# Optimization experiments

Hardware: AMD Instinct MI355X
Metric: run time of the kernel (lower is better)

The kernel has to match this reference:

```python
import jax, jax.numpy as jnp
import numpy as np

KNOWN_POINTS = 8
TAU = 1.0


def setup_inputs() -> dict:
    key = jax.random.key(0)
    k1, k2, k3 = jax.random.split(key, 3)
    B, N, H = 8, 56564, 256
    return {
        "x": jax.random.normal(k1, (B, N), dtype=jnp.float32),
        "point_weight": jax.random.normal(k2, (1, N), dtype=jnp.float32),
        "weight": jax.random.normal(k3, (1, N, H), dtype=jnp.float32),
        "bias": jnp.zeros((1, H), dtype=jnp.float32),
    }


def _softmax_point_selection(point_weight, B, tau):
    """Iterative straight-through HardSoftmax top-k selection (stage=2).
    Returns a (B, N) {0,1}-valued mask (with straight-through softmax grads)."""
    N = point_weight.shape[1]
    weights = jnp.broadcast_to(point_weight, (B, N))  # repeat_interleave over batch
    minimum = jax.lax.stop_gradient(jnp.min(weights))
    total = jnp.zeros((B, N), dtype=weights.dtype)
    for _ in range(KNOWN_POINTS):
        soft = jax.nn.softmax(weights / tau, axis=1)
        hard = jax.nn.one_hot(jnp.argmax(weights, axis=1), N, dtype=weights.dtype)
        # straight-through: forward = hard, backward = softmax jacobian
        one_hot = hard - jax.lax.stop_gradient(soft) + soft
        total = total + one_hot
        # masked_fill at selected positions (no grad through filled entries)
        weights = jnp.where(hard > 0, minimum - 10000.0, weights)
    return total


def reference(x, point_weight, weight, bias):
    B = x.shape[0]
    mask = _softmax_point_selection(point_weight, B, TAU)  # (B, N)
    # out[b,h] = sum_n x[b,n] * mask[b,n] * W[n,h] + bias[h]
    # (equivalent to masking the (B,N,H) weight then matmul, without materializing it)
    out = jnp.einsum('bn,nh->bh', x * mask, weight[0]) + bias
    return out
```

## Files before the change

kernel.cpp:

```cpp
#include <hip/hip_runtime.h>
#include <math.h>

#define TPB 256
#define KSEL 8
#define MAGIC 0x5EEDC0DEu

__device__ __forceinline__ unsigned long long make_key(float v, unsigned int idx) {
    unsigned int u = __float_as_uint(v);
    unsigned int ord = (u & 0x80000000u) ? ~u : (u | 0x80000000u);
    return ((unsigned long long)ord << 32) | (unsigned long long)(~idx);
}

__device__ __forceinline__ unsigned long long kmax(unsigned long long a, unsigned long long b) {
    return a > b ? a : b;
}

__device__ __forceinline__ unsigned long long wave_kmax(unsigned long long k) {
    #pragma unroll
    for (int o = 32; o > 0; o >>= 1) k = kmax(k, __shfl_xor(k, o, 64));
    return k;
}

__global__ __launch_bounds__(TPB) void fused_topk_linear(
        const float* __restrict__ x, const float* __restrict__ pw,
        const float* __restrict__ w, const float* __restrict__ bias,
        float* __restrict__ out,
        unsigned int* __restrict__ flags,
        unsigned long long* __restrict__ ws_keys,
        int N, int H, int B, int nblk) {
    __shared__ unsigned long long s_wk[(TPB / 64) * KSEL];
    __shared__ int s_idx[KSEL];
    __shared__ float s_x[16][KSEL];

    const int tid  = threadIdx.x;
    const int lane = tid & 63;
    const int wid  = tid >> 6;
    const int bid  = blockIdx.x;
    const int N4   = N >> 2;
    const int tailN = N - (N4 << 2);
    const int gid  = bid * TPB + tid;

    unsigned long long cand[5] = {0ull, 0ull, 0ull, 0ull, 0ull};
    if (gid < N4) {
        const float4 v = reinterpret_cast<const float4*>(pw)[gid];
        const unsigned int base = (unsigned int)gid * 4u;
        cand[0] = make_key(v.x, base + 0u);
        cand[1] = make_key(v.y, base + 1u);
        cand[2] = make_key(v.z, base + 2u);
        cand[3] = make_key(v.w, base + 3u);
    }
    if (bid == 0 && tid < tailN) {
        const unsigned int gi = (unsigned int)(N4 * 4 + tid);
        cand[4] = make_key(pw[gi], gi);
    }

    #pragma unroll 1
    for (int p = 0; p < KSEL; ++p) {
        unsigned long long k = kmax(kmax(kmax(cand[0], cand[1]), kmax(cand[2], cand[3])), cand[4]);
        k = wave_kmax(k);
        if (lane == 0) s_wk[wid * KSEL + p] = k;
        #pragma unroll
        for (int c = 0; c < 5; ++c) if (cand[c] == k) cand[c] = 0ull;
    }
    __syncthreads();

    if (wid == 0) {
        unsigned long long c0 = (lane < (TPB / 64) * KSEL) ? s_wk[lane] : 0ull;
        #pragma unroll 1
        for (int p = 0; p < KSEL; ++p) {
            unsigned long long m = wave_kmax(c0);
            if (lane == 0)
                __hip_atomic_store(&ws_keys[bid * KSEL + p], m,
                                   __ATOMIC_RELAXED, __HIP_MEMORY_SCOPE_AGENT);
            if (c0 == m) c0 = 0ull;
        }
        if (lane == 0 && bid != 0)
            __hip_atomic_store(&flags[bid], MAGIC,
                               __ATOMIC_RELEASE, __HIP_MEMORY_SCOPE_AGENT);
    }
    if (bid != 0) return;

    for (int i = 1 + tid; i < nblk; i += TPB) {
        while (__hip_atomic_load(&flags[i], __ATOMIC_ACQUIRE,
                                 __HIP_MEMORY_SCOPE_AGENT) != MAGIC)
            __builtin_amdgcn_s_sleep(1);
    }
    __syncthreads();

    const int nk = nblk * KSEL;
    const int k0i = wid * 128 + lane * 2;
    unsigned long long c0 = (k0i < nk)
        ? __hip_atomic_load(&ws_keys[k0i], __ATOMIC_RELAXED, __HIP_MEMORY_SCOPE_AGENT) : 0ull;
    unsigned long long c1 = (k0i + 1 < nk)
        ? __hip_atomic_load(&ws_keys[k0i + 1], __ATOMIC_RELAXED, __HIP_MEMORY_SCOPE_AGENT) : 0ull;
    #pragma unroll 1
    for (int p = 0; p < KSEL; ++p) {
        unsigned long long m = wave_kmax(kmax(c0, c1));
        if (lane == 0) s_wk[wid * KSEL + p] = m;
        if (c0 == m) c0 = 0ull;
        if (c1 == m) c1 = 0ull;
    }
    __syncthreads();
    if (wid == 0) {
        unsigned long long c = (lane < (TPB / 64) * KSEL) ? s_wk[lane] : 0ull;
        #pragma unroll 1
        for (int p = 0; p < KSEL; ++p) {
            unsigned long long m = wave_kmax(c);
            if (lane == 0) s_idx[p] = (int)(~(unsigned int)(m & 0xffffffffull));
            if (c == m) c = 0ull;
        }
    }
    __syncthreads();

    if (tid < B * KSEL) {
        const int b = tid >> 3, k = tid & 7;
        s_x[b][k] = x[(size_t)b * N + s_idx[k]];
    }
    __syncthreads();

    for (int h = tid; h < H; h += TPB) {
        float wv[KSEL];
        #pragma unroll
        for (int k = 0; k < KSEL; ++k) wv[k] = w[(size_t)s_idx[k] * H + h];
        const float bv = bias[h];
        for (int b = 0; b < B; ++b) {
            float acc = bv;
            #pragma unroll
            for (int k = 0; k < KSEL; ++k) acc += s_x[b][k] * wv[k];
            out[(size_t)b * H + h] = acc;
        }
    }
}

extern "C" void kernel_launch(void* const* d_in, const int* in_sizes, int n_in,
                              void* d_out, int out_size, void* d_ws, size_t ws_size,
                              hipStream_t stream) {
    const float* x    = (const float*)d_in[0];
    const float* pw   = (const float*)d_in[1];
    const float* w    = (const float*)d_in[2];
    const float* bias = (const float*)d_in[3];
    float* out = (float*)d_out;

    const int N = in_sizes[1];
    const int H = in_sizes[3];
    const int B = in_sizes[0] / N;
    const int N4 = N >> 2;
    const int nblk = (N4 + TPB - 1) / TPB;

    unsigned int* flags = (unsigned int*)d_ws;
    unsigned long long* keys = (unsigned long long*)((char*)d_ws + 512);

    fused_topk_linear<<<nblk, TPB, 0, stream>>>(x, pw, w, bias, out,
                                                flags, keys, N, H, B, nblk);
}
```

Before: 18.91 us.

## Replace iterative top-8 extraction with butterfly sorting-network merges and spread output over blocks

Replaces the eight sequential wave-max-and-remove passes with a per-thread sorted list of 8 candidates merged across the wave by a butterfly of bitonic top-8 merges, and the same merge across waves and across blocks. The final reduction now runs in the first B blocks, each computing one batch row, instead of block 0 doing all rows after waiting on every other block. This cuts serial shuffle rounds and shortens the tail on the last block. In exchange it adds register pressure from 8-wide u64 arrays, and B blocks now spin-wait on every flag. The final reduction also assumes nblk is at most 64 and that the flags are reset between launches.

```diff
diff --git a/kernel.cpp b/kernel.cpp
--- a/kernel.cpp
+++ b/kernel.cpp
@@ -5,20 +5,39 @@
 #define KSEL 8
 #define MAGIC 0x5EEDC0DEu
 
-__device__ __forceinline__ unsigned long long make_key(float v, unsigned int idx) {
+typedef unsigned long long u64;
+
+__device__ __forceinline__ u64 make_key(float v, unsigned int idx) {
     unsigned int u = __float_as_uint(v);
     unsigned int ord = (u & 0x80000000u) ? ~u : (u | 0x80000000u);
-    return ((unsigned long long)ord << 32) | (unsigned long long)(~idx);
+    return ((u64)ord << 32) | (u64)(~idx);
+}
+__device__ __forceinline__ u64 kmax(u64 a, u64 b) { return a > b ? a : b; }
+__device__ __forceinline__ void cswap(u64 &a, u64 &b) {
+    u64 hi = a > b ? a : b;
+    u64 lo = a > b ? b : a;
+    a = hi; b = lo;
 }
 
-__device__ __forceinline__ unsigned long long kmax(unsigned long long a, unsigned long long b) {
-    return a > b ? a : b;
+__device__ __forceinline__ void merge8(u64 a[8], const u64 b[8]) {
+    u64 t[8];
+    #pragma unroll
+    for (int i = 0; i < 8; ++i) t[i] = kmax(a[i], b[7 - i]);
+    cswap(t[0], t[4]); cswap(t[1], t[5]); cswap(t[2], t[6]); cswap(t[3], t[7]);
+    cswap(t[0], t[2]); cswap(t[1], t[3]); cswap(t[4], t[6]); cswap(t[5], t[7]);
+    cswap(t[0], t[1]); cswap(t[2], t[3]); cswap(t[4], t[5]); cswap(t[6], t[7]);
+    #pragma unroll
+    for (int i = 0; i < 8; ++i) a[i] = t[i];
 }
 
-__device__ __forceinline__ unsigned long long wave_kmax(unsigned long long k) {
+__device__ __forceinline__ void wave_butterfly_top8(u64 r[8]) {
     #pragma unroll
-    for (int o = 32; o > 0; o >>= 1) k = kmax(k, __shfl_xor(k, o, 64));
-    return k;
+    for (int o = 1; o < 64; o <<= 1) {
+        u64 b[8];
+        #pragma unroll
+        for (int i = 0; i < 8; ++i) b[i] = __shfl_xor(r[i], o, 64);
+        merge8(r, b);
+    }
 }
 
 __global__ __launch_bounds__(TPB) void fused_topk_linear(
@@ -26,11 +45,9 @@
         const float* __restrict__ w, const float* __restrict__ bias,
         float* __restrict__ out,
         unsigned int* __restrict__ flags,
-        unsigned long long* __restrict__ ws_keys,
+        u64* __restrict__ ws_keys,
         int N, int H, int B, int nblk) {
-    __shared__ unsigned long long s_wk[(TPB / 64) * KSEL];
-    __shared__ int s_idx[KSEL];
-    __shared__ float s_x[16][KSEL];
+    __shared__ u64 s_wk[TPB / 64][KSEL];
 
     const int tid  = threadIdx.x;
     const int lane = tid & 63;
@@ -40,95 +57,86 @@
     const int tailN = N - (N4 << 2);
     const int gid  = bid * TPB + tid;
 
-    unsigned long long cand[5] = {0ull, 0ull, 0ull, 0ull, 0ull};
-    if (gid < N4) {
-        const float4 v = reinterpret_cast<const float4*>(pw)[gid];
-        const unsigned int base = (unsigned int)gid * 4u;
-        cand[0] = make_key(v.x, base + 0u);
-        cand[1] = make_key(v.y, base + 1u);
-        cand[2] = make_key(v.z, base + 2u);
-        cand[3] = make_key(v.w, base + 3u);
-    }
-    if (bid == 0 && tid < tailN) {
-        const unsigned int gi = (unsigned int)(N4 * 4 + tid);
-        cand[4] = make_key(pw[gi], gi);
+    u64 r[8];
+    {
+        u64 c0 = 0, c1 = 0, c2 = 0, c3 = 0, c4 = 0;
+        if (gid < N4) {
+            const float4 v = reinterpret_cast<const float4*>(pw)[gid];
+            const unsigned int base = (unsigned int)gid * 4u;
+            c0 = make_key(v.x, base + 0u);
+            c1 = make_key(v.y, base + 1u);
+            c2 = make_key(v.z, base + 2u);
+            c3 = make_key(v.w, base + 3u);
+        }
+        if (bid == 0 && tid < tailN) {
+            const unsigned int gi = (unsigned int)(N4 * 4 + tid);
+            c4 = make_key(pw[gi], gi);
+        }
+        cswap(c0, c1); cswap(c3, c4); cswap(c2, c4); cswap(c2, c3); cswap(c0, c3);
+        cswap(c0, c2); cswap(c1, c4); cswap(c1, c3); cswap(c1, c2);
+        r[0] = c0; r[1] = c1; r[2] = c2; r[3] = c3; r[4] = c4;
+        r[5] = 0;  r[6] = 0;  r[7] = 0;
     }
 
-    #pragma unroll 1
-    for (int p = 0; p < KSEL; ++p) {
-        unsigned long long k = kmax(kmax(kmax(cand[0], cand[1]), kmax(cand[2], cand[3])), cand[4]);
-        k = wave_kmax(k);
-        if (lane == 0) s_wk[wid * KSEL + p] = k;
+    wave_butterfly_top8(r);
+
+    if (lane == 0) {
         #pragma unroll
-        for (int c = 0; c < 5; ++c) if (cand[c] == k) cand[c] = 0ull;
+        for (int i = 0; i < 8; ++i) s_wk[wid][i] = r[i];
     }
     __syncthreads();
-
     if (wid == 0) {
-        unsigned long long c0 = (lane < (TPB / 64) * KSEL) ? s_wk[lane] : 0ull;
-        #pragma unroll 1
-        for (int p = 0; p < KSEL; ++p) {
-            unsigned long long m = wave_kmax(c0);
-            if (lane == 0)
-                __hip_atomic_store(&ws_keys[bid * KSEL + p], m,
+        #pragma unroll
+        for (int wv = 1; wv < TPB / 64; ++wv) {
+            u64 b[8];
+            #pragma unroll
+            for (int i = 0; i < 8; ++i) b[i] = s_wk[wv][i];
+            merge8(r, b);
+        }
+        if (lane == 0) {
+            #pragma unroll
+            for (int i = 0; i < 8; ++i)
+                __hip_atomic_store(&ws_keys[bid * KSEL + i], r[i],
                                    __ATOMIC_RELAXED, __HIP_MEMORY_SCOPE_AGENT);
-            if (c0 == m) c0 = 0ull;
-        }
-        if (lane == 0 && bid != 0)
             __hip_atomic_store(&flags[bid], MAGIC,
                                __ATOMIC_RELEASE, __HIP_MEMORY_SCOPE_AGENT);
+        }
     }
-    if (bid != 0) return;
+    if (bid >= B) return;
 
-    for (int i = 1 + tid; i < nblk; i += TPB) {
+    for (int i = tid; i < nblk; i += TPB) {
         while (__hip_atomic_load(&flags[i], __ATOMIC_ACQUIRE,
                                  __HIP_MEMORY_SCOPE_AGENT) != MAGIC)
             __builtin_amdgcn_s_sleep(1);
     }
     __syncthreads();
 
-    const int nk = nblk * KSEL;
-    const int k0i = wid * 128 + lane * 2;
-    unsigned long long c0 = (k0i < nk)
-        ? __hip_atomic_load(&ws_keys[k0i], __ATOMIC_RELAXED, __HIP_MEMORY_SCOPE_AGENT) : 0ull;
-    unsigned long long c1 = (k0i + 1 < nk)
-        ? __hip_atomic_load(&ws_keys[k0i + 1], __ATOMIC_RELAXED, __HIP_MEMORY_SCOPE_AGENT) : 0ull;
-    #pragma unroll 1
-    for (int p = 0; p < KSEL; ++p) {
-        unsigned long long m = wave_kmax(kmax(c0, c1));
-        if (lane == 0) s_wk[wid * KSEL + p] = m;
-        if (c0 == m) c0 = 0ull;
-        if (c1 == m) c1 = 0ull;
+    u64 g[8];
+    if (lane < nblk) {
+        #pragma unroll
+        for (int i = 0; i < 8; ++i)
+            g[i] = __hip_atomic_load(&ws_keys[lane * KSEL + i],
+                                     __ATOMIC_RELAXED, __HIP_MEMORY_SCOPE_AGENT);
+    } else {
+        #pragma unroll
+        for (int i = 0; i < 8; ++i) g[i] = 0ull;
     }
-    __syncthreads();
-    if (wid == 0) {
-        unsigned long long c = (lane < (TPB / 64) * KSEL) ? s_wk[lane] : 0ull;
-        #pragma unroll 1
-        for (int p = 0; p < KSEL; ++p) {
-            unsigned long long m = wave_kmax(c);
-            if (lane == 0) s_idx[p] = (int)(~(unsigned int)(m & 0xffffffffull));
-            if (c == m) c = 0ull;
-        }
-    }
-    __syncthreads();
+    wave_butterfly_top8(g);
 
-    if (tid < B * KSEL) {
-        const int b = tid >> 3, k = tid & 7;
-        s_x[b][k] = x[(size_t)b * N + s_idx[k]];
-    }
-    __syncthreads();
+    int idx[KSEL];
+    #pragma unroll
+    for (int k = 0; k < KSEL; ++k)
+        idx[k] = __builtin_amdgcn_readfirstlane((int)(~(unsigned int)(g[k] & 0xffffffffull)));
 
+    const int b = bid;
+    float xv[KSEL];
+    #pragma unroll
+    for (int k = 0; k < KSEL; ++k) xv[k] = x[(size_t)b * N + idx[k]];
     for (int h = tid; h < H; h += TPB) {
-        float wv[KSEL];
+        float acc = bias[h];
         #pragma unroll
-        for (int k = 0; k < KSEL; ++k) wv[k] = w[(size_t)s_idx[k] * H + h];
-        const float bv = bias[h];
-        for (int b = 0; b < B; ++b) {
-            float acc = bv;
-            #pragma unroll
-            for (int k = 0; k < KSEL; ++k) acc += s_x[b][k] * wv[k];
-            out[(size_t)b * H + h] = acc;
-        }
+        for (int k = 0; k < KSEL; ++k) acc += xv[k] * w[(size_t)idx[k] * H + h];
+        out[(size_t)b * H + h] = acc;
     }
 }
 
@@ -148,7 +156,7 @@
     const int nblk = (N4 + TPB - 1) / TPB;
 
     unsigned int* flags = (unsigned int*)d_ws;
-    unsigned long long* keys = (unsigned long long*)((char*)d_ws + 512);
+    u64* keys = (u64*)((char*)d_ws + 512);
 
     fused_topk_linear<<<nblk, TPB, 0, stream>>>(x, pw, w, bias, out,
                                                 flags, keys, N, H, B, nblk);
```

After: 18.61 us. Within noise of the previous version (-1.6%).
